# Optimization experiments

Hardware: AMD Instinct MI355X
Metric: run time of the kernel (lower is better)

The kernel has to match this reference:

```python
import jax, jax.numpy as jnp
import numpy as np

DIM = 768
NUM_HEADS = 12
HEAD_DIM = DIM // NUM_HEADS
SCALE = HEAD_DIM ** (-0.5)


def setup_inputs() -> dict:
    key = jax.random.key(0)
    ks = jax.random.split(key, 8)
    B, Nq, Nk, Nv = 2, 2048, 2048, 2048
    init = 0.02
    return {
        "xq": jax.random.normal(ks[0], (B, Nq, DIM), dtype=jnp.float32),
        "xk": jax.random.normal(ks[1], (B, Nk, DIM), dtype=jnp.float32),
        "xv": jax.random.normal(ks[2], (B, Nv, DIM), dtype=jnp.float32),
        # torch nn.Linear weights are [out_features, in_features]; qkv_bias=False
        "Wq": jax.random.normal(ks[3], (DIM, DIM), dtype=jnp.float32) * init,
        "Wk": jax.random.normal(ks[4], (DIM, DIM), dtype=jnp.float32) * init,
        "Wv": jax.random.normal(ks[5], (DIM, DIM), dtype=jnp.float32) * init,
        "Wp": jax.random.normal(ks[6], (DIM, DIM), dtype=jnp.float32) * init,
        "bp": jax.random.normal(ks[7], (DIM,), dtype=jnp.float32) * init,
    }


def reference(xq, xk, xv, Wq, Wk, Wv, Wp, bp):
    B, Nq, C = xq.shape
    H, D = NUM_HEADS, HEAD_DIM
    # linear projections (torch Linear: x @ W.T), split heads -> [B, H, N, D]
    q = (xq @ Wq.T).reshape(B, Nq, H, D).transpose(0, 2, 1, 3)
    k = (xk @ Wk.T).reshape(B, xk.shape[1], H, D).transpose(0, 2, 1, 3)
    v = (xv @ Wv.T).reshape(B, xv.shape[1], H, D).transpose(0, 2, 1, 3)
    # attention scores [B, H, Nq, Nk]
    attn = jnp.einsum("bhqd,bhkd->bhqk", q, k) * SCALE
    attn = jax.nn.softmax(attn, axis=-1)
    # weighted values -> merge heads [B, Nq, C]
    out = jnp.einsum("bhqk,bhkd->bhqd", attn, v)
    out = out.transpose(0, 2, 1, 3).reshape(B, Nq, C)
    return out @ Wp.T + bp
```

## Files before the change

kernel.cpp:

```cpp
#include <hip/hip_runtime.h>
#include <hip/hip_bf16.h>


#define NSEQ 2048
#define CDIM 768
#define NH   12
#define HD   64
#define MTOT 4096
#define XEL  (MTOT*CDIM)
#define WEL  (CDIM*CDIM)
#define X8   (XEL/8)
#define W8   (WEL/8)
#define PSTR 72
#define QSCALE 0.18033688011112042f

typedef __attribute__((ext_vector_type(8))) short bf16x8;
typedef __attribute__((ext_vector_type(4))) float floatx4;

static __device__ __forceinline__ unsigned short f2bf(float f) {
  union { float f; unsigned int u; } v; v.f = f;
  return (unsigned short)((v.u + 0x8000u) >> 16);
}
static __device__ __forceinline__ unsigned pk2bf(float a, float b) {
  unsigned ua = __float_as_uint(a) + 0x8000u;
  unsigned ub = __float_as_uint(b) + 0x8000u;
  return __builtin_amdgcn_perm(ub, ua, 0x07060302);
}

static __device__ __forceinline__ void lds16(const void* g, void* l) {
  __builtin_amdgcn_global_load_lds(
      (const __attribute__((address_space(1))) unsigned int*)g,
      (__attribute__((address_space(3))) unsigned int*)l, 16, 0, 0);
}

__global__ __launch_bounds__(256) void cast_all(
    const float* __restrict__ xq, const float* __restrict__ xk,
    const float* __restrict__ xv, const float* __restrict__ wq,
    const float* __restrict__ wk, const float* __restrict__ wv,
    const float* __restrict__ wp,
    unsigned short* __restrict__ Xq, unsigned short* __restrict__ Xk,
    unsigned short* __restrict__ Xv, unsigned short* __restrict__ Wq,
    unsigned short* __restrict__ Wk, unsigned short* __restrict__ Wv,
    unsigned short* __restrict__ Wp) {
  int i = blockIdx.x * 256 + threadIdx.x;
  const float* s; unsigned short* d; int off;
  if (i < 3 * X8) {
    int t = i / X8; off = i - t * X8;
    s = (t == 0) ? xq : (t == 1) ? xk : xv;
    d = (t == 0) ? Xq : (t == 1) ? Xk : Xv;
  } else {
    int j = i - 3 * X8; int t = j / W8; off = j - t * W8;
    s = (t == 0) ? wq : (t == 1) ? wk : (t == 2) ? wv : wp;
    d = (t == 0) ? Wq : (t == 1) ? Wk : (t == 2) ? Wv : Wp;
  }
  const float4* sp = (const float4*)s + (size_t)off * 2;
  float4 a = sp[0], b = sp[1];
  uint4 o;
  o.x = pk2bf(a.x, a.y); o.y = pk2bf(a.z, a.w);
  o.z = pk2bf(b.x, b.y); o.w = pk2bf(b.z, b.w);
  *(uint4*)(d + (size_t)off * 8) = o;
}

__global__ __launch_bounds__(256) void gemm_qkv(
    const unsigned short* __restrict__ Xq, const unsigned short* __restrict__ Xk,
    const unsigned short* __restrict__ Xv, const unsigned short* __restrict__ Wq,
    const unsigned short* __restrict__ Wk, const unsigned short* __restrict__ Wv,
    unsigned short* __restrict__ Qo, unsigned short* __restrict__ Ko,
    unsigned short* __restrict__ Vo) {
  int z = blockIdx.z;
  const unsigned short* A; const unsigned short* B; int am0, bn0, RA;
  if (z == 0)      { A = Xq; B = Wq; am0 = blockIdx.y * 128; bn0 = blockIdx.x * 96; RA = 128; }
  else if (z == 1) { A = Xk; B = Wk; am0 = blockIdx.y * 128; bn0 = blockIdx.x * 96; RA = 128; }
  else             { A = Wv; B = Xv; am0 = blockIdx.x * 96;  bn0 = blockIdx.y * 128; RA = 96; }
  __shared__ __align__(16) unsigned short S[224 * 64];
  int tid = threadIdx.x, lane = tid & 63, wave = tid >> 6;
  int quad = lane >> 4, l15 = lane & 15, l7 = l15 & 7;

  const unsigned short* gptr[7]; int ldo[7];
#pragma unroll
  for (int i = 0; i < 7; i++) {
    int idx = i * 256 + tid;
    int row = idx >> 3, c = (idx & 7) ^ (row & 7);
    gptr[i] = (row < RA ? A + (size_t)(am0 + row) * CDIM
                        : B + (size_t)(bn0 + row - RA) * CDIM) + c * 8;
    ldo[i] = idx * 8;
  }
  floatx4 acc[12];
#pragma unroll
  for (int i = 0; i < 12; i++) acc[i] = (floatx4){0.f, 0.f, 0.f, 0.f};

  for (int k0 = 0; k0 < CDIM; k0 += 64) {
#pragma unroll
    for (int i = 0; i < 7; i++) lds16(gptr[i] + k0, &S[ldo[i]]);
    __syncthreads();
    if (z < 2) {
      int wm = (wave >> 1) * 64, wn = (wave & 1) * 48;
#pragma unroll
      for (int ks = 0; ks < 2; ks++) {
        int csw = ((ks * 4 + quad) ^ l7) * 8;
        bf16x8 af[4], bfr[3];
#pragma unroll
        for (int i = 0; i < 4; i++)
          af[i] = *(const bf16x8*)&S[(wm + i * 16 + l15) * 64 + csw];
#pragma unroll
        for (int j = 0; j < 3; j++)
          bfr[j] = *(const bf16x8*)&S[(128 + wn + j * 16 + l15) * 64 + csw];
#pragma unroll
        for (int mi = 0; mi < 4; mi++)
#pragma unroll
          for (int ni = 0; ni < 3; ni++)
            acc[mi * 3 + ni] = __builtin_amdgcn_mfma_f32_16x16x32_bf16(
                af[mi], bfr[ni], acc[mi * 3 + ni], 0, 0, 0);
      }
    } else {
      int wm = (wave & 1) * 48, wn = (wave >> 1) * 64;
#pragma unroll
      for (int ks = 0; ks < 2; ks++) {
        int csw = ((ks * 4 + quad) ^ l7) * 8;
        bf16x8 af[3], bfr[4];
#pragma unroll
        for (int i = 0; i < 3; i++)
          af[i] = *(const bf16x8*)&S[(wm + i * 16 + l15) * 64 + csw];
#pragma unroll
        for (int j = 0; j < 4; j++)
          bfr[j] = *(const bf16x8*)&S[(96 + wn + j * 16 + l15) * 64 + csw];
#pragma unroll
        for (int mi = 0; mi < 3; mi++)
#pragma unroll
          for (int ni = 0; ni < 4; ni++)
            acc[mi * 4 + ni] = __builtin_amdgcn_mfma_f32_16x16x32_bf16(
                af[mi], bfr[ni], acc[mi * 4 + ni], 0, 0, 0);
      }
    }
    __syncthreads();
  }
  if (z < 2) {
    int wm = (wave >> 1) * 64, wn = (wave & 1) * 48;
#pragma unroll
    for (int mi = 0; mi < 4; mi++)
#pragma unroll
      for (int ni = 0; ni < 3; ni++)
#pragma unroll
        for (int r = 0; r < 4; r++) {
          int grow = am0 + wm + mi * 16 + quad * 4 + r;
          int gcol = bn0 + wn + ni * 16 + l15;
          float v = acc[mi * 3 + ni][r];
          int b = grow >> 11, nq = grow & 2047, h = gcol >> 6, dd = gcol & 63;
          if (z == 0)
            Qo[((size_t)(b * NH + h) * NSEQ + nq) * HD + dd] = f2bf(v * QSCALE);
          else
            Ko[((size_t)(b * NH + h) * NSEQ + nq) * HD + dd] = f2bf(v);
        }
  } else {
    int wm = (wave & 1) * 48, wn = (wave >> 1) * 64;
#pragma unroll
    for (int mi = 0; mi < 3; mi++)
#pragma unroll
      for (int ni = 0; ni < 4; ni++)
#pragma unroll
        for (int r = 0; r < 4; r++) {
          int o = am0 + wm + mi * 16 + quad * 4 + r;
          int mg = bn0 + wn + ni * 16 + l15;
          int b = mg >> 11, nq = mg & 2047;
          Vo[((size_t)b * CDIM + o) * NSEQ + nq] = f2bf(acc[mi * 4 + ni][r]);
        }
  }
}

__global__ __launch_bounds__(256, 3) void attn_kernel(
    const unsigned short* __restrict__ Q, const unsigned short* __restrict__ K,
    const unsigned short* __restrict__ Vt, unsigned short* __restrict__ ctx) {
  int qt = blockIdx.x, bh = blockIdx.y;
  int tid = threadIdx.x, lane = tid & 63, wave = tid >> 6;
  int half = wave >> 1, qsub = wave & 1;
  int quad = lane >> 4, l15 = lane & 15, l7 = l15 & 7;
  __shared__ __align__(16) unsigned short Ks[2][64 * 64];
  __shared__ __align__(16) unsigned short Vs[2][64 * 64];
  __shared__ __align__(16) unsigned short Ps[4][16 * PSTR];

  const unsigned short* Qg = Q + ((size_t)bh * NSEQ + qt * 64 + qsub * 32) * HD;
  const unsigned short* Kg = K + ((size_t)bh * NSEQ + half * 1024) * HD;
  const unsigned short* Vg = Vt + (size_t)bh * HD * NSEQ + half * 1024;

  bf16x8 qf[2][2];
#pragma unroll
  for (int qi = 0; qi < 2; qi++)
#pragma unroll
    for (int ks = 0; ks < 2; ks++)
      qf[qi][ks] = *(const bf16x8*)(Qg + (qi * 16 + l15) * HD + ks * 32 + quad * 8);

  bf16x8 ones;
#pragma unroll
  for (int i = 0; i < 8; i++) ones[i] = (short)0x3F80;

  int tid2 = tid & 127;
  int kgo[4], vgo[4], ldst[4];
#pragma unroll
  for (int i = 0; i < 4; i++) {
    int idx = i * 128 + tid2;
    int R = idx >> 3, c = (idx & 7) ^ (R & 7);
    kgo[i] = R * HD + c * 8;
    vgo[i] = R * NSEQ + c * 8;
    ldst[i] = idx * 8;
  }
  unsigned short* Ksh = Ks[half];
  unsigned short* Vsh = Vs[half];
  unsigned short* Pw = &Ps[wave][0];

  floatx4 ol[2];
  floatx4 o[2][4];
#pragma unroll
  for (int qi = 0; qi < 2; qi++) {
    ol[qi] = (floatx4){0.f, 0.f, 0.f, 0.f};
#pragma unroll
    for (int dt = 0; dt < 4; dt++) o[qi][dt] = (floatx4){0.f, 0.f, 0.f, 0.f};
  }

  for (int t = 0; t < 16; t++) {
    int k0 = t * 64;
#pragma unroll
    for (int i = 0; i < 4; i++) {
      lds16(Kg + (size_t)k0 * HD + kgo[i], &Ksh[ldst[i]]);
      lds16(Vg + k0 + vgo[i], &Vsh[ldst[i]]);
    }
    __syncthreads();
    bf16x8 kf[4][2], vf[4][2];
#pragma unroll
    for (int nt = 0; nt < 4; nt++)
#pragma unroll
      for (int x = 0; x < 2; x++)
        kf[nt][x] = *(const bf16x8*)&Ksh[(nt * 16 + l15) * 64 + ((x * 4 + quad) ^ l7) * 8];
#pragma unroll
    for (int dt = 0; dt < 4; dt++)
#pragma unroll
      for (int x = 0; x < 2; x++)
        vf[dt][x] = *(const bf16x8*)&Vsh[(dt * 16 + l15) * 64 + ((x * 4 + quad) ^ l7) * 8];
#pragma unroll
    for (int qi = 0; qi < 2; qi++) {
#pragma unroll
      for (int nt = 0; nt < 4; nt++) {
        floatx4 st = (floatx4){0.f, 0.f, 0.f, 0.f};
        st = __builtin_amdgcn_mfma_f32_16x16x32_bf16(kf[nt][0], qf[qi][0], st, 0, 0, 0);
        st = __builtin_amdgcn_mfma_f32_16x16x32_bf16(kf[nt][1], qf[qi][1], st, 0, 0, 0);
        float p0 = __builtin_exp2f(st[0]), p1 = __builtin_exp2f(st[1]);
        float p2 = __builtin_exp2f(st[2]), p3 = __builtin_exp2f(st[3]);
        *(uint2*)&Pw[l15 * PSTR + nt * 16 + quad * 4] =
            make_uint2(pk2bf(p0, p1), pk2bf(p2, p3));
      }
#pragma unroll
      for (int ks = 0; ks < 2; ks++) {
        bf16x8 pf = *(const bf16x8*)&Pw[l15 * PSTR + ks * 32 + quad * 8];
        ol[qi] = __builtin_amdgcn_mfma_f32_16x16x32_bf16(ones, pf, ol[qi], 0, 0, 0);
#pragma unroll
        for (int dt = 0; dt < 4; dt++)
          o[qi][dt] = __builtin_amdgcn_mfma_f32_16x16x32_bf16(vf[dt][ks], pf, o[qi][dt], 0, 0, 0);
      }
    }
    __syncthreads();
  }
  float* Obuf = (float*)&Ks[0][0];
  float* Lbuf = (float*)&Ps[0][0];
  if (half == 1) {
#pragma unroll
    for (int qi = 0; qi < 2; qi++) {
      int ro = qsub * 32 + qi * 16 + l15;
#pragma unroll
      for (int dt = 0; dt < 4; dt++)
        *(floatx4*)&Obuf[ro * 64 + dt * 16 + quad * 4] = o[qi][dt];
      if (quad == 0) Lbuf[ro] = ol[qi][0];
    }
  }
  __syncthreads();
  if (half == 0) {
    int b = bh / NH, h = bh - b * NH;
#pragma unroll
    for (int qi = 0; qi < 2; qi++) {
      int ro = qsub * 32 + qi * 16 + l15;
      float inv = 1.f / (ol[qi][0] + Lbuf[ro]);
      int qrow = qt * 64 + ro;
      size_t gbase = (size_t)(b * NSEQ + qrow) * CDIM + h * HD + quad * 4;
#pragma unroll
      for (int dt = 0; dt < 4; dt++) {
        floatx4 ob = *(floatx4*)&Obuf[ro * 64 + dt * 16 + quad * 4];
        float v0 = (o[qi][dt][0] + ob[0]) * inv, v1 = (o[qi][dt][1] + ob[1]) * inv;
        float v2 = (o[qi][dt][2] + ob[2]) * inv, v3 = (o[qi][dt][3] + ob[3]) * inv;
        *(uint2*)&ctx[gbase + dt * 16] = make_uint2(pk2bf(v0, v1), pk2bf(v2, v3));
      }
    }
  }
}

__global__ __launch_bounds__(256) void gemm_out(
    const unsigned short* __restrict__ A, const unsigned short* __restrict__ B,
    const float* __restrict__ bias, float* __restrict__ out) {
  int m0 = blockIdx.y * 64, n0 = blockIdx.x * 64;
  __shared__ __align__(16) unsigned short As[64 * 128];
  __shared__ __align__(16) unsigned short Bs[64 * 128];
  int tid = threadIdx.x, lane = tid & 63, wave = tid >> 6;
  int quad = lane >> 4, l15 = lane & 15, l7 = l15 & 7;
  int wm = (wave >> 1) * 32, wn = (wave & 1) * 32;
  floatx4 acc[2][2];
#pragma unroll
  for (int i = 0; i < 2; i++)
#pragma unroll
    for (int j = 0; j < 2; j++) acc[i][j] = (floatx4){0.f, 0.f, 0.f, 0.f};

  for (int k0 = 0; k0 < CDIM; k0 += 128) {
#pragma unroll
    for (int i = 0; i < 4; i++) {
      int idx = i * 256 + tid;
      int R = idx >> 4, c4 = idx & 15;
      int cs = (c4 & 8) | ((c4 & 7) ^ (R & 7));
      lds16(A + (size_t)(m0 + R) * CDIM + k0 + cs * 8, &As[idx * 8]);
      lds16(B + (size_t)(n0 + R) * CDIM + k0 + cs * 8, &Bs[idx * 8]);
    }
    __syncthreads();
#pragma unroll
    for (int ks = 0; ks < 4; ks++) {
      int c = ks * 4 + quad;
      int csw = ((c & 8) | ((c & 7) ^ l7)) * 8;
      bf16x8 af[2], bfr[2];
#pragma unroll
      for (int i = 0; i < 2; i++)
        af[i] = *(const bf16x8*)&As[(wm + i * 16 + l15) * 128 + csw];
#pragma unroll
      for (int i = 0; i < 2; i++)
        bfr[i] = *(const bf16x8*)&Bs[(wn + i * 16 + l15) * 128 + csw];
#pragma unroll
      for (int mi = 0; mi < 2; mi++)
#pragma unroll
        for (int ni = 0; ni < 2; ni++)
          acc[mi][ni] = __builtin_amdgcn_mfma_f32_16x16x32_bf16(
              af[mi], bfr[ni], acc[mi][ni], 0, 0, 0);
    }
    __syncthreads();
  }
  float bv[2];
#pragma unroll
  for (int ni = 0; ni < 2; ni++) bv[ni] = bias[n0 + wn + ni * 16 + l15];
#pragma unroll
  for (int mi = 0; mi < 2; mi++)
#pragma unroll
    for (int ni = 0; ni < 2; ni++)
#pragma unroll
      for (int r = 0; r < 4; r++) {
        int grow = m0 + wm + mi * 16 + quad * 4 + r;
        int gcol = n0 + wn + ni * 16 + l15;
        out[(size_t)grow * CDIM + gcol] = acc[mi][ni][r] + bv[ni];
      }
}

extern "C" void kernel_launch(void* const* d_in, const int* in_sizes, int n_in,
                              void* d_out, int out_size, void* d_ws, size_t ws_size,
                              hipStream_t stream) {
  const float* xq = (const float*)d_in[0];
  const float* xk = (const float*)d_in[1];
  const float* xv = (const float*)d_in[2];
  const float* wq = (const float*)d_in[3];
  const float* wk = (const float*)d_in[4];
  const float* wv = (const float*)d_in[5];
  const float* wp = (const float*)d_in[6];
  const float* bp = (const float*)d_in[7];
  float* out = (float*)d_out;

  char* p = (char*)d_ws;
  unsigned short* Xq = (unsigned short*)p; p += (size_t)XEL * 2;
  unsigned short* Xk = (unsigned short*)p; p += (size_t)XEL * 2;
  unsigned short* Xv = (unsigned short*)p; p += (size_t)XEL * 2;
  unsigned short* Wq = (unsigned short*)p; p += (size_t)WEL * 2;
  unsigned short* Wk = (unsigned short*)p; p += (size_t)WEL * 2;
  unsigned short* Wv = (unsigned short*)p; p += (size_t)WEL * 2;
  unsigned short* Wp = (unsigned short*)p; p += (size_t)WEL * 2;
  unsigned short* Qb = (unsigned short*)p; p += (size_t)XEL * 2;
  unsigned short* Kb = (unsigned short*)p; p += (size_t)XEL * 2;
  unsigned short* Vb = (unsigned short*)p; p += (size_t)XEL * 2;
  unsigned short* Cx = (unsigned short*)p; p += (size_t)XEL * 2;

  cast_all<<<(3 * X8 + 4 * W8) / 256, 256, 0, stream>>>(
      xq, xk, xv, wq, wk, wv, wp, Xq, Xk, Xv, Wq, Wk, Wv, Wp);

  gemm_qkv<<<dim3(8, 32, 3), 256, 0, stream>>>(
      Xq, Xk, Xv, Wq, Wk, Wv, Qb, Kb, Vb);

  attn_kernel<<<dim3(NSEQ / 64, 2 * NH), 256, 0, stream>>>(Qb, Kb, Vb, Cx);

  gemm_out<<<dim3(CDIM / 64, MTOT / 64), 256, 0, stream>>>(Cx, Wp, bp, out);
}
```

Before: 192.2 us.

## Split keys across all four waves and load K/V straight from global

Each wave now covers all 64 query rows of the tile and walks its own quarter of the keys (512). K and V fragments are read directly from global memory into registers, which removes the LDS staging and the per-tile __syncthreads. The row sum is accumulated in scalar registers and reduced with shuffles, replacing the ones-matrix MFMA. Partial outputs are combined through shared memory in a two-stage tree, and the 1D grid is remapped so blocks of the same head are spread out, probably for L2/XCD locality. The cost is many uncoalesced global loads and higher register pressure from the 4x4 output accumulators.

Measured after the change: 215.1 us. 1.12x slower.

```diff
diff --git a/kernel.cpp b/kernel.cpp
--- a/kernel.cpp
+++ b/kernel.cpp
@@ -170,73 +170,44 @@
 __global__ __launch_bounds__(256, 3) void attn_kernel(
     const unsigned short* __restrict__ Q, const unsigned short* __restrict__ K,
     const unsigned short* __restrict__ Vt, unsigned short* __restrict__ ctx) {
-  int qt = blockIdx.x, bh = blockIdx.y;
+  int n = blockIdx.x;
+  int g = n >> 3;
+  int bh = (n & 7) * 3 + (g >> 5);
+  int qt = g & 31;
   int tid = threadIdx.x, lane = tid & 63, wave = tid >> 6;
-  int half = wave >> 1, qsub = wave & 1;
-  int quad = lane >> 4, l15 = lane & 15, l7 = l15 & 7;
-  __shared__ __align__(16) unsigned short Ks[2][64 * 64];
-  __shared__ __align__(16) unsigned short Vs[2][64 * 64];
-  __shared__ __align__(16) unsigned short Ps[4][16 * PSTR];
-
-  const unsigned short* Qg = Q + ((size_t)bh * NSEQ + qt * 64 + qsub * 32) * HD;
-  const unsigned short* Kg = K + ((size_t)bh * NSEQ + half * 1024) * HD;
-  const unsigned short* Vg = Vt + (size_t)bh * HD * NSEQ + half * 1024;
-
-  bf16x8 qf[2][2];
-#pragma unroll
-  for (int qi = 0; qi < 2; qi++)
+  int quad = lane >> 4, l15 = lane & 15;
+  __shared__ __align__(16) unsigned short SH[4 * 64 * PSTR];
+
+  const unsigned short* Qg = Q + ((size_t)bh * NSEQ + qt * 64) * HD;
+  const unsigned short* Kg = K + ((size_t)bh * NSEQ + wave * 512) * HD;
+  const unsigned short* Vg = Vt + (size_t)bh * HD * NSEQ + wave * 512;
+
+  bf16x8 qf[4][2];
+#pragma unroll
+  for (int qi = 0; qi < 4; qi++)
 #pragma unroll
     for (int ks = 0; ks < 2; ks++)
       qf[qi][ks] = *(const bf16x8*)(Qg + (qi * 16 + l15) * HD + ks * 32 + quad * 8);
 
-  bf16x8 ones;
-#pragma unroll
-  for (int i = 0; i < 8; i++) ones[i] = (short)0x3F80;
-
-  int tid2 = tid & 127;
-  int kgo[4], vgo[4], ldst[4];
-#pragma unroll
-  for (int i = 0; i < 4; i++) {
-    int idx = i * 128 + tid2;
-    int R = idx >> 3, c = (idx & 7) ^ (R & 7);
-    kgo[i] = R * HD + c * 8;
-    vgo[i] = R * NSEQ + c * 8;
-    ldst[i] = idx * 8;
-  }
-  unsigned short* Ksh = Ks[half];
-  unsigned short* Vsh = Vs[half];
-  unsigned short* Pw = &Ps[wave][0];
-
-  floatx4 ol[2];
-  floatx4 o[2][4];
-#pragma unroll
-  for (int qi = 0; qi < 2; qi++) {
-    ol[qi] = (floatx4){0.f, 0.f, 0.f, 0.f};
+  unsigned short* Pw = &SH[wave * 64 * PSTR];
+  float lacc[4] = {0.f, 0.f, 0.f, 0.f};
+  floatx4 o[4][4];
+#pragma unroll
+  for (int qi = 0; qi < 4; qi++)
 #pragma unroll
     for (int dt = 0; dt < 4; dt++) o[qi][dt] = (floatx4){0.f, 0.f, 0.f, 0.f};
-  }
-
-  for (int t = 0; t < 16; t++) {
-    int k0 = t * 64;
-#pragma unroll
-    for (int i = 0; i < 4; i++) {
-      lds16(Kg + (size_t)k0 * HD + kgo[i], &Ksh[ldst[i]]);
-      lds16(Vg + k0 + vgo[i], &Vsh[ldst[i]]);
-    }
-    __syncthreads();
-    bf16x8 kf[4][2], vf[4][2];
+
+  for (int t = 0; t < 8; t++) {
+    const unsigned short* Kt = Kg + t * 64 * HD;
+    const unsigned short* Vp = Vg + t * 64;
+    bf16x8 kf[4][2];
 #pragma unroll
     for (int nt = 0; nt < 4; nt++)
 #pragma unroll
       for (int x = 0; x < 2; x++)
-        kf[nt][x] = *(const bf16x8*)&Ksh[(nt * 16 + l15) * 64 + ((x * 4 + quad) ^ l7) * 8];
-#pragma unroll
-    for (int dt = 0; dt < 4; dt++)
-#pragma unroll
-      for (int x = 0; x < 2; x++)
-        vf[dt][x] = *(const bf16x8*)&Vsh[(dt * 16 + l15) * 64 + ((x * 4 + quad) ^ l7) * 8];
-#pragma unroll
-    for (int qi = 0; qi < 2; qi++) {
+        kf[nt][x] = *(const bf16x8*)(Kt + (nt * 16 + l15) * HD + x * 32 + quad * 8);
+#pragma unroll
+    for (int qi = 0; qi < 4; qi++)
 #pragma unroll
       for (int nt = 0; nt < 4; nt++) {
         floatx4 st = (floatx4){0.f, 0.f, 0.f, 0.f};
@@ -244,44 +215,87 @@
         st = __builtin_amdgcn_mfma_f32_16x16x32_bf16(kf[nt][1], qf[qi][1], st, 0, 0, 0);
         float p0 = __builtin_exp2f(st[0]), p1 = __builtin_exp2f(st[1]);
         float p2 = __builtin_exp2f(st[2]), p3 = __builtin_exp2f(st[3]);
-        *(uint2*)&Pw[l15 * PSTR + nt * 16 + quad * 4] =
+        lacc[qi] += (p0 + p1) + (p2 + p3);
+        *(uint2*)&Pw[(qi * 16 + l15) * PSTR + nt * 16 + quad * 4] =
             make_uint2(pk2bf(p0, p1), pk2bf(p2, p3));
       }
+    bf16x8 vf[4][2];
+#pragma unroll
+    for (int dt = 0; dt < 4; dt++)
+#pragma unroll
+      for (int x = 0; x < 2; x++)
+        vf[dt][x] = *(const bf16x8*)(Vp + (dt * 16 + l15) * NSEQ + x * 32 + quad * 8);
+#pragma unroll
+    for (int qi = 0; qi < 4; qi++)
 #pragma unroll
       for (int ks = 0; ks < 2; ks++) {
-        bf16x8 pf = *(const bf16x8*)&Pw[l15 * PSTR + ks * 32 + quad * 8];
-        ol[qi] = __builtin_amdgcn_mfma_f32_16x16x32_bf16(ones, pf, ol[qi], 0, 0, 0);
+        bf16x8 pf = *(const bf16x8*)&Pw[(qi * 16 + l15) * PSTR + ks * 32 + quad * 8];
 #pragma unroll
         for (int dt = 0; dt < 4; dt++)
           o[qi][dt] = __builtin_amdgcn_mfma_f32_16x16x32_bf16(vf[dt][ks], pf, o[qi][dt], 0, 0, 0);
       }
-    }
-    __syncthreads();
-  }
-  float* Obuf = (float*)&Ks[0][0];
-  float* Lbuf = (float*)&Ps[0][0];
-  if (half == 1) {
-#pragma unroll
-    for (int qi = 0; qi < 2; qi++) {
-      int ro = qsub * 32 + qi * 16 + l15;
+  }
+#pragma unroll
+  for (int qi = 0; qi < 4; qi++) {
+    lacc[qi] += __shfl_xor(lacc[qi], 16, 64);
+    lacc[qi] += __shfl_xor(lacc[qi], 32, 64);
+  }
+  float* Ob0 = (float*)&SH[0];
+  float* Ob1 = (float*)&SH[8192];
+  float* Lb0 = (float*)&SH[16384];
+  float* Lb1 = (float*)&SH[16512];
+  __syncthreads();
+  if (wave == 1 || wave == 3) {
+    float* Ob = (wave == 1) ? Ob0 : Ob1;
+    float* Lb = (wave == 1) ? Lb0 : Lb1;
+#pragma unroll
+    for (int qi = 0; qi < 4; qi++) {
+      int ro = qi * 16 + l15;
 #pragma unroll
       for (int dt = 0; dt < 4; dt++)
-        *(floatx4*)&Obuf[ro * 64 + dt * 16 + quad * 4] = o[qi][dt];
-      if (quad == 0) Lbuf[ro] = ol[qi][0];
+        *(floatx4*)&Ob[ro * 64 + dt * 16 + quad * 4] = o[qi][dt];
+      if (quad == 0) Lb[ro] = lacc[qi];
     }
   }
   __syncthreads();
-  if (half == 0) {
+  if (wave == 0 || wave == 2) {
+    float* Ob = (wave == 0) ? Ob0 : Ob1;
+    float* Lb = (wave == 0) ? Lb0 : Lb1;
+#pragma unroll
+    for (int qi = 0; qi < 4; qi++) {
+      int ro = qi * 16 + l15;
+#pragma unroll
+      for (int dt = 0; dt < 4; dt++) {
+        floatx4 ob = *(floatx4*)&Ob[ro * 64 + dt * 16 + quad * 4];
+        o[qi][dt][0] += ob[0]; o[qi][dt][1] += ob[1];
+        o[qi][dt][2] += ob[2]; o[qi][dt][3] += ob[3];
+      }
+      lacc[qi] += Lb[ro];
+    }
+  }
+  __syncthreads();
+  if (wave == 2) {
+#pragma unroll
+    for (int qi = 0; qi < 4; qi++) {
+      int ro = qi * 16 + l15;
+#pragma unroll
+      for (int dt = 0; dt < 4; dt++)
+        *(floatx4*)&Ob0[ro * 64 + dt * 16 + quad * 4] = o[qi][dt];
+      if (quad == 0) Lb0[ro] = lacc[qi];
+    }
+  }
+  __syncthreads();
+  if (wave == 0) {
     int b = bh / NH, h = bh - b * NH;
 #pragma unroll
-    for (int qi = 0; qi < 2; qi++) {
-      int ro = qsub * 32 + qi * 16 + l15;
-      float inv = 1.f / (ol[qi][0] + Lbuf[ro]);
+    for (int qi = 0; qi < 4; qi++) {
+      int ro = qi * 16 + l15;
+      float inv = 1.f / (lacc[qi] + Lb0[ro]);
       int qrow = qt * 64 + ro;
       size_t gbase = (size_t)(b * NSEQ + qrow) * CDIM + h * HD + quad * 4;
 #pragma unroll
       for (int dt = 0; dt < 4; dt++) {
-        floatx4 ob = *(floatx4*)&Obuf[ro * 64 + dt * 16 + quad * 4];
+        floatx4 ob = *(floatx4*)&Ob0[ro * 64 + dt * 16 + quad * 4];
         float v0 = (o[qi][dt][0] + ob[0]) * inv, v1 = (o[qi][dt][1] + ob[1]) * inv;
         float v2 = (o[qi][dt][2] + ob[2]) * inv, v3 = (o[qi][dt][3] + ob[3]) * inv;
         *(uint2*)&ctx[gbase + dt * 16] = make_uint2(pk2bf(v0, v1), pk2bf(v2, v3));
@@ -382,7 +396,7 @@
   gemm_qkv<<<dim3(8, 32, 3), 256, 0, stream>>>(
       Xq, Xk, Xv, Wq, Wk, Wv, Qb, Kb, Vb);
 
-  attn_kernel<<<dim3(NSEQ / 64, 2 * NH), 256, 0, stream>>>(Qb, Kb, Vb, Cx);
+  attn_kernel<<<768, 256, 0, stream>>>(Qb, Kb, Vb, Cx);
 
   gemm_out<<<dim3(CDIM / 64, MTOT / 64), 256, 0, stream>>>(Cx, Wp, bp, out);
 }
```

## Remap block indices for XCD-local L2 reuse and widen output GEMM tiles

Applied to the files above, without the earlier changes.

Replaces the 2D/3D grids of the QKV GEMM, the attention kernel and the output GEMM with 1D grids. Block IDs are decoded so that blocks landing on the same XCD (round-robin by blockIdx mod 8) share the same rows or heads, which is meant to improve L2 hit rates on MI355X's split L2. The output GEMM also moves from 64x64 to 64x96 tiles with a single shared LDS buffer, giving 512 blocks instead of 768 and more B reuse per block. The risks are fewer blocks in the output GEMM and more LDS use per block.

After: 186.2 us. 3.1% less time.

```diff
diff --git a/kernel.cpp b/kernel.cpp
--- a/kernel.cpp
+++ b/kernel.cpp
@@ -67,11 +67,15 @@
     const unsigned short* __restrict__ Wk, const unsigned short* __restrict__ Wv,
     unsigned short* __restrict__ Qo, unsigned short* __restrict__ Ko,
     unsigned short* __restrict__ Vo) {
-  int z = blockIdx.z;
+  int i0 = blockIdx.x;
+  int mg = i0 & 7; int t0 = i0 >> 3;
+  int z = t0 % 3; int u = t0 / 3;
+  int xn = u & 7, ysub = u >> 3;
+  int y = mg * 4 + ysub;
   const unsigned short* A; const unsigned short* B; int am0, bn0, RA;
-  if (z == 0)      { A = Xq; B = Wq; am0 = blockIdx.y * 128; bn0 = blockIdx.x * 96; RA = 128; }
-  else if (z == 1) { A = Xk; B = Wk; am0 = blockIdx.y * 128; bn0 = blockIdx.x * 96; RA = 128; }
-  else             { A = Wv; B = Xv; am0 = blockIdx.x * 96;  bn0 = blockIdx.y * 128; RA = 96; }
+  if (z == 0)      { A = Xq; B = Wq; am0 = y * 128; bn0 = xn * 96; RA = 128; }
+  else if (z == 1) { A = Xk; B = Wk; am0 = y * 128; bn0 = xn * 96; RA = 128; }
+  else             { A = Wv; B = Xv; am0 = xn * 96; bn0 = y * 128; RA = 96; }
   __shared__ __align__(16) unsigned short S[224 * 64];
   int tid = threadIdx.x, lane = tid & 63, wave = tid >> 6;
   int quad = lane >> 4, l15 = lane & 15, l7 = l15 & 7;
@@ -160,8 +164,8 @@
 #pragma unroll
         for (int r = 0; r < 4; r++) {
           int o = am0 + wm + mi * 16 + quad * 4 + r;
-          int mg = bn0 + wn + ni * 16 + l15;
-          int b = mg >> 11, nq = mg & 2047;
+          int mgl = bn0 + wn + ni * 16 + l15;
+          int b = mgl >> 11, nq = mgl & 2047;
           Vo[((size_t)b * CDIM + o) * NSEQ + nq] = f2bf(acc[mi * 4 + ni][r]);
         }
   }
@@ -170,7 +174,10 @@
 __global__ __launch_bounds__(256, 3) void attn_kernel(
     const unsigned short* __restrict__ Q, const unsigned short* __restrict__ K,
     const unsigned short* __restrict__ Vt, unsigned short* __restrict__ ctx) {
-  int qt = blockIdx.x, bh = blockIdx.y;
+  int i0 = blockIdx.x;
+  int xcd = i0 & 7; int t0 = i0 >> 3;
+  int bh = xcd * 3 + (t0 >> 5);
+  int qt = t0 & 31;
   int tid = threadIdx.x, lane = tid & 63, wave = tid >> 6;
   int half = wave >> 1, qsub = wave & 1;
   int quad = lane >> 4, l15 = lane & 15, l7 = l15 & 7;
@@ -293,60 +300,61 @@
 __global__ __launch_bounds__(256) void gemm_out(
     const unsigned short* __restrict__ A, const unsigned short* __restrict__ B,
     const float* __restrict__ bias, float* __restrict__ out) {
-  int m0 = blockIdx.y * 64, n0 = blockIdx.x * 64;
-  __shared__ __align__(16) unsigned short As[64 * 128];
-  __shared__ __align__(16) unsigned short Bs[64 * 128];
+  int i0 = blockIdx.x;
+  int mg = i0 & 7; int t0 = i0 >> 3;
+  int n0 = (t0 & 7) * 96;
+  int m0 = (mg * 8 + (t0 >> 3)) * 64;
+  __shared__ __align__(16) unsigned short S[160 * 128];
   int tid = threadIdx.x, lane = tid & 63, wave = tid >> 6;
   int quad = lane >> 4, l15 = lane & 15, l7 = l15 & 7;
-  int wm = (wave >> 1) * 32, wn = (wave & 1) * 32;
-  floatx4 acc[2][2];
-#pragma unroll
-  for (int i = 0; i < 2; i++)
-#pragma unroll
-    for (int j = 0; j < 2; j++) acc[i][j] = (floatx4){0.f, 0.f, 0.f, 0.f};
+  int wm = (wave >> 1) * 32, wn = (wave & 1) * 48;
+  floatx4 acc[6];
+#pragma unroll
+  for (int i = 0; i < 6; i++) acc[i] = (floatx4){0.f, 0.f, 0.f, 0.f};
 
   for (int k0 = 0; k0 < CDIM; k0 += 128) {
 #pragma unroll
-    for (int i = 0; i < 4; i++) {
+    for (int i = 0; i < 10; i++) {
       int idx = i * 256 + tid;
       int R = idx >> 4, c4 = idx & 15;
       int cs = (c4 & 8) | ((c4 & 7) ^ (R & 7));
-      lds16(A + (size_t)(m0 + R) * CDIM + k0 + cs * 8, &As[idx * 8]);
-      lds16(B + (size_t)(n0 + R) * CDIM + k0 + cs * 8, &Bs[idx * 8]);
+      const unsigned short* g = (R < 64)
+          ? A + (size_t)(m0 + R) * CDIM : B + (size_t)(n0 + R - 64) * CDIM;
+      lds16(g + k0 + cs * 8, &S[idx * 8]);
     }
     __syncthreads();
 #pragma unroll
     for (int ks = 0; ks < 4; ks++) {
       int c = ks * 4 + quad;
       int csw = ((c & 8) | ((c & 7) ^ l7)) * 8;
-      bf16x8 af[2], bfr[2];
+      bf16x8 af[2], bfr[3];
 #pragma unroll
       for (int i = 0; i < 2; i++)
-        af[i] = *(const bf16x8*)&As[(wm + i * 16 + l15) * 128 + csw];
-#pragma unroll
-      for (int i = 0; i < 2; i++)
-        bfr[i] = *(const bf16x8*)&Bs[(wn + i * 16 + l15) * 128 + csw];
+        af[i] = *(const bf16x8*)&S[(wm + i * 16 + l15) * 128 + csw];
+#pragma unroll
+      for (int j = 0; j < 3; j++)
+        bfr[j] = *(const bf16x8*)&S[(64 + wn + j * 16 + l15) * 128 + csw];
 #pragma unroll
       for (int mi = 0; mi < 2; mi++)
 #pragma unroll
-        for (int ni = 0; ni < 2; ni++)
-          acc[mi][ni] = __builtin_amdgcn_mfma_f32_16x16x32_bf16(
-              af[mi], bfr[ni], acc[mi][ni], 0, 0, 0);
-    }
-    __syncthreads();
-  }
-  float bv[2];
-#pragma unroll
-  for (int ni = 0; ni < 2; ni++) bv[ni] = bias[n0 + wn + ni * 16 + l15];
+        for (int ni = 0; ni < 3; ni++)
+          acc[mi * 3 + ni] = __builtin_amdgcn_mfma_f32_16x16x32_bf16(
+              af[mi], bfr[ni], acc[mi * 3 + ni], 0, 0, 0);
+    }
+    __syncthreads();
+  }
+  float bv[3];
+#pragma unroll
+  for (int ni = 0; ni < 3; ni++) bv[ni] = bias[n0 + wn + ni * 16 + l15];
 #pragma unroll
   for (int mi = 0; mi < 2; mi++)
 #pragma unroll
-    for (int ni = 0; ni < 2; ni++)
+    for (int ni = 0; ni < 3; ni++)
 #pragma unroll
       for (int r = 0; r < 4; r++) {
         int grow = m0 + wm + mi * 16 + quad * 4 + r;
         int gcol = n0 + wn + ni * 16 + l15;
-        out[(size_t)grow * CDIM + gcol] = acc[mi][ni][r] + bv[ni];
+        out[(size_t)grow * CDIM + gcol] = acc[mi * 3 + ni][r] + bv[ni];
       }
 }
 
@@ -379,10 +387,10 @@
   cast_all<<<(3 * X8 + 4 * W8) / 256, 256, 0, stream>>>(
       xq, xk, xv, wq, wk, wv, wp, Xq, Xk, Xv, Wq, Wk, Wv, Wp);
 
-  gemm_qkv<<<dim3(8, 32, 3), 256, 0, stream>>>(
+  gemm_qkv<<<768, 256, 0, stream>>>(
       Xq, Xk, Xv, Wq, Wk, Wv, Qb, Kb, Vb);
 
-  attn_kernel<<<dim3(NSEQ / 64, 2 * NH), 256, 0, stream>>>(Qb, Kb, Vb, Cx);
-
-  gemm_out<<<dim3(CDIM / 64, MTOT / 64), 256, 0, stream>>>(Cx, Wp, bp, out);
-}
+  attn_kernel<<<768, 256, 0, stream>>>(Qb, Kb, Vb, Cx);
+
+  gemm_out<<<512, 256, 0, stream>>>(Cx, Wp, bp, out);
+}
```
